# Kernel tuning notes

Hardware: AMD Instinct MI355X
Metric: run time of the kernel (lower is better)

The kernel has to match this reference:

```python
import jax, jax.numpy as jnp
import numpy as np

HEADS = 4
KNN = 32
N_KEYS = 512
K_DIM = 512
HALF = K_DIM // 2
V_DIM = 1024
IN_DIM = 1024


def setup_inputs() -> dict:
    key = jax.random.key(0)
    k1, k2, k3, k4, k5 = jax.random.split(key, 5)
    x = jax.random.normal(k1, (1, 2048, IN_DIM), dtype=jnp.float32)
    w_q = jax.random.normal(k2, (HEADS * K_DIM, IN_DIM), dtype=jnp.float32) * (IN_DIM ** -0.5)
    b_q = jax.random.normal(k3, (HEADS * K_DIM,), dtype=jnp.float32) * 0.01
    # subkeys: uniform(-1/sqrt(half), 1/sqrt(half)) as in get_uniform_keys
    bound = 1.0 / np.sqrt(HALF)
    keys = jax.random.uniform(k4, (HEADS, 2, N_KEYS, HALF), dtype=jnp.float32,
                              minval=-bound, maxval=bound)
    # values: normal(0, v_dim**-0.5)
    values = jax.random.normal(k5, (N_KEYS * N_KEYS, V_DIM), dtype=jnp.float32) * (V_DIM ** -0.5)
    return {"x": x, "w_q": w_q, "b_q": b_q, "keys": keys, "values": values}


def reference(x, w_q, b_q, keys, values):
    B, S, D = x.shape
    bs = B * S
    # query projection: (bs, heads*k_dim) -> (bs, heads, 2, half)
    q = (x.reshape(bs, D) @ w_q.T + b_q).reshape(bs, HEADS, 2, HALF)
    # per-head, per-half subkey scores: (bs, heads, 2, n_keys)
    scores = jnp.einsum('bhtd,htnd->bhtn', q, keys)
    s_top, i_top = jax.lax.top_k(scores, KNN)          # (bs, heads, 2, knn)
    s1, s2 = s_top[:, :, 0], s_top[:, :, 1]
    i1, i2 = i_top[:, :, 0], i_top[:, :, 1]
    # cross-product of the two half top-k sets: (bs, heads, knn*knn)
    all_s = (s1[..., :, None] + s2[..., None, :]).reshape(bs, HEADS, KNN * KNN)
    all_i = (i1[..., :, None] * N_KEYS + i2[..., None, :]).reshape(bs, HEADS, KNN * KNN)
    best_s, best_pos = jax.lax.top_k(all_s, KNN)       # (bs, heads, knn)
    idx = jnp.take_along_axis(all_i, best_pos, axis=-1)
    # softmax over knn per head (matches softmax on scores.view(-1, knn))
    w = jax.nn.softmax(best_s, axis=-1).reshape(bs, HEADS * KNN)
    idx = idx.reshape(bs, HEADS * KNN)
    # weighted EmbeddingBag gather-sum over the value table
    out = jnp.einsum('bk,bkd->bd', w, values[idx])     # (bs, v_dim)
    return out.reshape(B, S, V_DIM)
```

## Files before the change

### kernel.cpp

```cpp
#include <hip/hip_runtime.h>
#include <math.h>

#define BSZ   2048
#define INDIM 1024
#define QDIM  2048
#define NHT   8
#define NKEYS 512
#define HALFD 256
#define KNN   32
#define VDIM  1024
#define HEADS 4

typedef _Float16 v8h __attribute__((ext_vector_type(8)));
typedef _Float16 v4h __attribute__((ext_vector_type(4)));
typedef float    v4f __attribute__((ext_vector_type(4)));

template<int KSHIFT, bool ASIDE>
__global__ __launch_bounds__(256) void split_kernel(
    const float* __restrict__ in, _Float16* __restrict__ out, int total4) {
  const int i = blockIdx.x * 256 + threadIdx.x;
  if (i >= total4) return;
  const long e0 = (long)i * 4;
  const int K = 1 << KSHIFT;
  const long r = e0 >> KSHIFT;
  const int k = (int)(e0 & (K - 1));
  const float4 a = *(const float4*)&in[e0];
  const float av[4] = {a.x, a.y, a.z, a.w};
  v4h hv, dv, mv;
  #pragma unroll
  for (int u = 0; u < 4; ++u) {
    const _Float16 hh = (_Float16)av[u];
    hv[u] = hh;
    mv[u] = (_Float16)((av[u] - (float)hh) * 64.0f);
    dv[u] = (_Float16)((float)hh * 0.015625f);
  }
  _Float16* base = out + r * (3L * K) + k;
  *(v4h*)(base)         = hv;
  *(v4h*)(base + K)     = ASIDE ? dv : mv;
  *(v4h*)(base + 2 * K) = ASIDE ? mv : dv;
}

__device__ __forceinline__ void gload16(const _Float16* g, _Float16* l) {
  __builtin_amdgcn_global_load_lds(
      (const __attribute__((address_space(1))) unsigned int*)g,
      (__attribute__((address_space(3))) unsigned int*)l, 16, 0, 0);
}

template<bool Q_EPI>
__global__ __launch_bounds__(256) void mfma_gemm(
    const _Float16* __restrict__ A, int lda, long aBS,
    const _Float16* __restrict__ B, int ldb, long bBS,
    const float* __restrict__ bias,
    float* __restrict__ Cf, int ldc, long cBS,
    _Float16* __restrict__ Cq, int K) {
  extern __shared__ __align__(16) char smem[];
  _Float16* Asm = (_Float16*)smem;
  _Float16* Bsm = (_Float16*)(smem + 16384);
  const int t = threadIdx.x;
  const int z = blockIdx.z;
  const _Float16* Ab = A + (size_t)z * aBS;
  const _Float16* Bb = B + (size_t)z * bBS;
  const int m0 = blockIdx.y * 128, n0 = blockIdx.x * 128;

  const int o0 = t * 16;
  const int os = o0 ^ (((o0 >> 7) & 3) << 4);
  const int sr = os >> 6;
  const int sk = (os & 63) >> 1;
  const _Float16* gA0 = Ab + (size_t)(m0 + sr) * lda + sk;
  const _Float16* gA1 = Ab + (size_t)(m0 + sr + 64) * lda + sk;
  const _Float16* gB0 = Bb + (size_t)(n0 + sr) * ldb + sk;
  const _Float16* gB1 = Bb + (size_t)(n0 + sr + 64) * ldb + sk;

  const int lane = t & 63, w = t >> 6;
  const int wr = (w >> 1) * 64, wc = (w & 1) * 64;
  const int fr = lane & 15, kg = lane >> 4;

  int aoff[4], boff[4];
  #pragma unroll
  for (int i = 0; i < 4; ++i) {
    const int ra = wr + i * 16 + fr;
    aoff[i] = (ra * 64 + ((kg ^ ((ra >> 1) & 3)) * 16)) >> 1;
    const int rb = wc + i * 16 + fr;
    boff[i] = (rb * 64 + ((kg ^ ((rb >> 1) & 3)) * 16)) >> 1;
  }

  v4f acc[4][4];
  #pragma unroll
  for (int i = 0; i < 4; ++i)
    #pragma unroll
    for (int j = 0; j < 4; ++j)
      acc[i][j] = (v4f){0.f, 0.f, 0.f, 0.f};

  gload16(gA0, Asm + t * 8);
  gload16(gA1, Asm + 2048 + t * 8);
  gload16(gB0, Bsm + t * 8);
  gload16(gB1, Bsm + 2048 + t * 8);
  __syncthreads();

  int cur = 0;
  for (int kt = 0; kt < K; kt += 32) {
    const int nxt = cur ^ 1;
    if (kt + 32 < K) {
      gload16(gA0 + kt + 32, Asm + nxt * 4096 + t * 8);
      gload16(gA1 + kt + 32, Asm + nxt * 4096 + 2048 + t * 8);
      gload16(gB0 + kt + 32, Bsm + nxt * 4096 + t * 8);
      gload16(gB1 + kt + 32, Bsm + nxt * 4096 + 2048 + t * 8);
    }
    v8h af[4], bf[4];
    #pragma unroll
    for (int i = 0; i < 4; ++i) af[i] = *(const v8h*)(Asm + cur * 4096 + aoff[i]);
    #pragma unroll
    for (int j = 0; j < 4; ++j) bf[j] = *(const v8h*)(Bsm + cur * 4096 + boff[j]);
    #pragma unroll
    for (int i = 0; i < 4; ++i)
      #pragma unroll
      for (int j = 0; j < 4; ++j)
        acc[i][j] = __builtin_amdgcn_mfma_f32_16x16x32_f16(af[i], bf[j], acc[i][j], 0, 0, 0);
    __syncthreads();
    cur = nxt;
  }

  if (Q_EPI) {
    float* Ct = (float*)smem;
    #pragma unroll
    for (int half = 0; half < 2; ++half) {
      __syncthreads();
      if ((w & 1) == half) {
        #pragma unroll
        for (int j = 0; j < 4; ++j) {
          const int colq = j * 16 + fr;
          const float bv = bias[n0 + half * 64 + colq];
          #pragma unroll
          for (int i = 0; i < 4; ++i)
            #pragma unroll
            for (int rr = 0; rr < 4; ++rr)
              Ct[(wr + i * 16 + kg * 4 + rr) * 68 + colq] = acc[i][j][rr] + bv;
        }
      }
      __syncthreads();
      const int r = t >> 1, cb = (t & 1) * 32;
      const int gcol = n0 + half * 64 + cb;
      const int ht = gcol >> 8, dd = gcol & 255;
      _Float16* p = Cq + (size_t)(m0 + r) * (3 * HALFD * NHT) + ht * (3 * HALFD) + dd;
      #pragma unroll
      for (int u = 0; u < 32; u += 8) {
        float vv[8];
        *(float4*)&vv[0] = *(const float4*)&Ct[r * 68 + cb + u];
        *(float4*)&vv[4] = *(const float4*)&Ct[r * 68 + cb + u + 4];
        v8h hv, dv, mv;
        #pragma unroll
        for (int e = 0; e < 8; ++e) {
          const _Float16 hh = (_Float16)vv[e];
          hv[e] = hh;
          mv[e] = (_Float16)((vv[e] - (float)hh) * 64.0f);
          dv[e] = (_Float16)((float)hh * 0.015625f);
        }
        *(v8h*)(p + u) = hv;
        *(v8h*)(p + HALFD + u) = dv;
        *(v8h*)(p + 2 * HALFD + u) = mv;
      }
    }
  } else {
    float* Cb = Cf + (size_t)z * cBS;
    #pragma unroll
    for (int i = 0; i < 4; ++i)
      #pragma unroll
      for (int j = 0; j < 4; ++j)
        #pragma unroll
        for (int rr = 0; rr < 4; ++rr) {
          const int rowg = m0 + wr + i * 16 + kg * 4 + rr;
          const int colg = n0 + wc + j * 16 + fr;
          Cb[(size_t)rowg * ldc + colg] = acc[i][j][rr];
        }
  }
}

__global__ __launch_bounds__(64) void topk1_kernel(
    const float* __restrict__ S, float* __restrict__ sTop, int* __restrict__ iTop) {
  const int row = blockIdx.x;
  const int lane = threadIdx.x;
  const float* sr = S + (size_t)row * NKEYS;
  float v[8];
  #pragma unroll
  for (int j = 0; j < 8; ++j) v[j] = sr[j * 64 + lane];
  for (int r = 0; r < KNN; ++r) {
    float bv = -INFINITY; int bi = 0x7fffffff;
    #pragma unroll
    for (int j = 0; j < 8; ++j) {
      int idx = j * 64 + lane;
      if (v[j] > bv) { bv = v[j]; bi = idx; }
    }
    #pragma unroll
    for (int off = 32; off > 0; off >>= 1) {
      float ov = __shfl_xor(bv, off);
      int oi = __shfl_xor(bi, off);
      if (ov > bv || (ov == bv && oi < bi)) { bv = ov; bi = oi; }
    }
    if (lane == 0) { sTop[(size_t)row * KNN + r] = bv; iTop[(size_t)row * KNN + r] = bi; }
    const int jj = bi >> 6;
    const bool mine = (bi & 63) == lane;
    #pragma unroll
    for (int j = 0; j < 8; ++j)
      if (mine && j == jj) v[j] = -INFINITY;
  }
}

__global__ __launch_bounds__(64) void topk2_kernel(
    const float* __restrict__ sTop, const int* __restrict__ iTop,
    float* __restrict__ wOut, int* __restrict__ idxOut) {
  const int row = blockIdx.x;
  const int lane = threadIdx.x;
  __shared__ float ls1[32], ls2[32], sel_s[32];
  __shared__ int li1[32], li2[32], sel_i[32];
  if (lane < 32) {
    ls1[lane] = sTop[(size_t)(2 * row) * KNN + lane];
    li1[lane] = iTop[(size_t)(2 * row) * KNN + lane];
    ls2[lane] = sTop[(size_t)(2 * row + 1) * KNN + lane];
    li2[lane] = iTop[(size_t)(2 * row + 1) * KNN + lane];
  }
  __syncthreads();
  float v[16];
  #pragma unroll
  for (int c = 0; c < 16; ++c) {
    int p = c * 64 + lane;
    v[c] = ls1[p >> 5] + ls2[p & 31];
  }
  for (int r = 0; r < KNN; ++r) {
    float bv = -INFINITY; int bp = 0x7fffffff;
    #pragma unroll
    for (int c = 0; c < 16; ++c) {
      int p = c * 64 + lane;
      if (v[c] > bv) { bv = v[c]; bp = p; }
    }
    #pragma unroll
    for (int off = 32; off > 0; off >>= 1) {
      float ov = __shfl_xor(bv, off);
      int op = __shfl_xor(bp, off);
      if (ov > bv || (ov == bv && op < bp)) { bv = ov; bp = op; }
    }
    if (lane == 0) {
      sel_s[r] = bv;
      sel_i[r] = li1[bp >> 5] * NKEYS + li2[bp & 31];
    }
    const int cc = bp >> 6;
    const bool mine = (bp & 63) == lane;
    #pragma unroll
    for (int c = 0; c < 16; ++c)
      if (mine && c == cc) v[c] = -INFINITY;
  }
  __syncthreads();
  const float m = sel_s[0];
  float e = (lane < 32) ? expf(sel_s[lane] - m) : 0.0f;
  float s = e;
  #pragma unroll
  for (int off = 32; off > 0; off >>= 1) s += __shfl_xor(s, off);
  if (lane < 32) {
    wOut[(size_t)row * KNN + lane] = e / s;
    idxOut[(size_t)row * KNN + lane] = sel_i[lane];
  }
}

__global__ __launch_bounds__(256) void gather_kernel(
    const float* __restrict__ values, const float* __restrict__ w,
    const int* __restrict__ idx, float* __restrict__ out) {
  const int b = blockIdx.x;
  const int tid = threadIdx.x;
  __shared__ float lw[128];
  __shared__ int lidx[128];
  if (tid < 128) {
    lw[tid] = w[(size_t)b * 128 + tid];
    lidx[tid] = idx[(size_t)b * 128 + tid];
  }
  __syncthreads();
  const int d0 = tid * 4;
  float4 acc = {0.f, 0.f, 0.f, 0.f};
  #pragma unroll 8
  for (int k = 0; k < 128; ++k) {
    const float4 vv = *(const float4*)&values[(size_t)lidx[k] * VDIM + d0];
    const float ww = lw[k];
    acc.x = fmaf(ww, vv.x, acc.x);
    acc.y = fmaf(ww, vv.y, acc.y);
    acc.z = fmaf(ww, vv.z, acc.z);
    acc.w = fmaf(ww, vv.w, acc.w);
  }
  *(float4*)&out[(size_t)b * VDIM + d0] = acc;
}

extern "C" void kernel_launch(void* const* d_in, const int* in_sizes, int n_in,
                              void* d_out, int out_size, void* d_ws, size_t ws_size,
                              hipStream_t stream) {
  const float* x      = (const float*)d_in[0];
  const float* w_q    = (const float*)d_in[1];
  const float* b_q    = (const float*)d_in[2];
  const float* keys   = (const float*)d_in[3];
  const float* values = (const float*)d_in[4];
  float* out = (float*)d_out;

  char* ws = (char*)d_ws;
  _Float16* xs    = (_Float16*)(ws);
  _Float16* wqs   = (_Float16*)(ws + (16u  << 20));
  _Float16* keyss = (_Float16*)(ws + (32u  << 20));
  _Float16* Qs    = (_Float16*)(ws + (40u  << 20));
  float*    S     = (float*)   (ws + (68u  << 20));
  float*    sTop  = (float*)   (ws + (100u << 20));
  int*      iTop  = (int*)     (ws + (102u << 20));
  float*    wF    = (float*)   (ws + (104u << 20));
  int*      idxF  = (int*)     (ws + (105u << 20));

  split_kernel<10, true ><<<2048, 256, 0, stream>>>(x,    xs,    524288);
  split_kernel<10, false><<<2048, 256, 0, stream>>>(w_q,  wqs,   524288);
  split_kernel<8,  false><<<1024, 256, 0, stream>>>(keys, keyss, 262144);

  mfma_gemm<true><<<dim3(QDIM / 128, BSZ / 128, 1), 256, 34816, stream>>>(
      xs, 3 * INDIM, 0, wqs, 3 * INDIM, 0, b_q,
      nullptr, 0, 0, Qs, 3 * INDIM);
  mfma_gemm<false><<<dim3(NKEYS / 128, BSZ / 128, NHT), 256, 32768, stream>>>(
      Qs, 3 * HALFD * NHT, 3 * HALFD, keyss, 3 * HALFD, (long)NKEYS * 3 * HALFD, nullptr,
      S, NHT * NKEYS, NKEYS, nullptr, 3 * HALFD);

  topk1_kernel<<<BSZ * NHT, 64, 0, stream>>>(S, sTop, iTop);
  topk2_kernel<<<BSZ * HEADS, 64, 0, stream>>>(sTop, iTop, wF, idxF);
  gather_kernel<<<BSZ, 256, 0, stream>>>(values, wF, idxF, out);
}
```

Measured before the change: 412.6 us.

## Fuse splits, widen GEMM K-tile, fuse score GEMM with top-k and top-k2 with gather

Merges the three fp16 split launches into one kernel. The query GEMM moves to a 64-wide K tile with an 8-way swizzle. The score GEMM becomes a 64x512 tile per block whose results stay in LDS and feed a per-row top-k there, so the full score matrix is never written to or read back from global memory. The second top-k, softmax and weighted gather now run in one kernel per token with four heads per block. This cuts launches and intermediate traffic, at the cost of very large LDS use (over 144 KB per block), which limits occupancy in the fused score kernel.

Result: slower. 468.1 us (+13.4%).

```diff
diff --git a/kernel.cpp b/kernel.cpp
--- a/kernel.cpp
+++ b/kernel.cpp
@@ -16,10 +16,8 @@
 typedef float    v4f __attribute__((ext_vector_type(4)));
 
 template<int KSHIFT, bool ASIDE>
-__global__ __launch_bounds__(256) void split_kernel(
-    const float* __restrict__ in, _Float16* __restrict__ out, int total4) {
-  const int i = blockIdx.x * 256 + threadIdx.x;
-  if (i >= total4) return;
+__device__ __forceinline__ void split4(const float* __restrict__ in,
+                                       _Float16* __restrict__ out, int i) {
   const long e0 = (long)i * 4;
   const int K = 1 << KSHIFT;
   const long r = e0 >> KSHIFT;
@@ -40,49 +38,55 @@
   *(v4h*)(base + 2 * K) = ASIDE ? mv : dv;
 }
 
+__global__ __launch_bounds__(256) void split_all_kernel(
+    const float* __restrict__ x, const float* __restrict__ wq, const float* __restrict__ ky,
+    _Float16* __restrict__ xs, _Float16* __restrict__ wqs, _Float16* __restrict__ kys) {
+  const int i = blockIdx.x * 256 + threadIdx.x;
+  if (i < 524288)            split4<10, true >(x,  xs,  i);
+  else if (i < 1048576)      split4<10, false>(wq, wqs, i - 524288);
+  else                       split4<8,  false>(ky, kys, i - 1048576);
+}
+
 __device__ __forceinline__ void gload16(const _Float16* g, _Float16* l) {
   __builtin_amdgcn_global_load_lds(
       (const __attribute__((address_space(1))) unsigned int*)g,
       (__attribute__((address_space(3))) unsigned int*)l, 16, 0, 0);
 }
 
-template<bool Q_EPI>
-__global__ __launch_bounds__(256) void mfma_gemm(
-    const _Float16* __restrict__ A, int lda, long aBS,
-    const _Float16* __restrict__ B, int ldb, long bBS,
-    const float* __restrict__ bias,
-    float* __restrict__ Cf, int ldc, long cBS,
-    _Float16* __restrict__ Cq, int K) {
-  extern __shared__ __align__(16) char smem[];
-  _Float16* Asm = (_Float16*)smem;
-  _Float16* Bsm = (_Float16*)(smem + 16384);
+__global__ __launch_bounds__(256) void gemm1_kernel(
+    const _Float16* __restrict__ A, const _Float16* __restrict__ B,
+    const float* __restrict__ bias, _Float16* __restrict__ Cq) {
+  __shared__ __align__(16) char smem[65536];
+  _Float16* sh = (_Float16*)smem;
   const int t = threadIdx.x;
-  const int z = blockIdx.z;
-  const _Float16* Ab = A + (size_t)z * aBS;
-  const _Float16* Bb = B + (size_t)z * bBS;
   const int m0 = blockIdx.y * 128, n0 = blockIdx.x * 128;
-
-  const int o0 = t * 16;
-  const int os = o0 ^ (((o0 >> 7) & 3) << 4);
-  const int sr = os >> 6;
-  const int sk = (os & 63) >> 1;
-  const _Float16* gA0 = Ab + (size_t)(m0 + sr) * lda + sk;
-  const _Float16* gA1 = Ab + (size_t)(m0 + sr + 64) * lda + sk;
-  const _Float16* gB0 = Bb + (size_t)(n0 + sr) * ldb + sk;
-  const _Float16* gB1 = Bb + (size_t)(n0 + sr + 64) * ldb + sk;
-
   const int lane = t & 63, w = t >> 6;
   const int wr = (w >> 1) * 64, wc = (w & 1) * 64;
   const int fr = lane & 15, kg = lane >> 4;
 
-  int aoff[4], boff[4];
-  #pragma unroll
-  for (int i = 0; i < 4; ++i) {
-    const int ra = wr + i * 16 + fr;
-    aoff[i] = (ra * 64 + ((kg ^ ((ra >> 1) & 3)) * 16)) >> 1;
-    const int rb = wc + i * 16 + fr;
-    boff[i] = (rb * 64 + ((kg ^ ((rb >> 1) & 3)) * 16)) >> 1;
-  }
+  const _Float16* gA[4]; const _Float16* gB[4];
+  int dA[4], dB[4];
+  #pragma unroll
+  for (int p = 0; p < 4; ++p) {
+    const int O = p * 4096 + t * 16;
+    const int os = O ^ (((O >> 7) & 7) << 4);
+    const int srow = os >> 7, sk = (os & 127) >> 1;
+    gA[p] = A + (size_t)(m0 + srow) * 3072 + sk;
+    gB[p] = B + (size_t)(n0 + srow) * 3072 + sk;
+    dA[p] = O >> 1;
+    dB[p] = (16384 + O) >> 1;
+  }
+
+  int aof[2][4], bof[2][4];
+  #pragma unroll
+  for (int ks = 0; ks < 2; ++ks)
+    #pragma unroll
+    for (int i = 0; i < 4; ++i) {
+      const int ra = wr + i * 16 + fr;
+      aof[ks][i] = (ra * 128 + ((((ks << 2) | kg) ^ (fr & 7)) << 4)) >> 1;
+      const int rb = wc + i * 16 + fr;
+      bof[ks][i] = ((rb * 128 + ((((ks << 2) | kg) ^ (fr & 7)) << 4)) >> 1) + 8192;
+    }
 
   v4f acc[4][4];
   #pragma unroll
@@ -91,156 +95,236 @@
     for (int j = 0; j < 4; ++j)
       acc[i][j] = (v4f){0.f, 0.f, 0.f, 0.f};
 
-  gload16(gA0, Asm + t * 8);
-  gload16(gA1, Asm + 2048 + t * 8);
-  gload16(gB0, Bsm + t * 8);
-  gload16(gB1, Bsm + 2048 + t * 8);
+  #pragma unroll
+  for (int p = 0; p < 4; ++p) { gload16(gA[p], sh + dA[p]); gload16(gB[p], sh + dB[p]); }
   __syncthreads();
 
   int cur = 0;
-  for (int kt = 0; kt < K; kt += 32) {
-    const int nxt = cur ^ 1;
-    if (kt + 32 < K) {
-      gload16(gA0 + kt + 32, Asm + nxt * 4096 + t * 8);
-      gload16(gA1 + kt + 32, Asm + nxt * 4096 + 2048 + t * 8);
-      gload16(gB0 + kt + 32, Bsm + nxt * 4096 + t * 8);
-      gload16(gB1 + kt + 32, Bsm + nxt * 4096 + 2048 + t * 8);
-    }
-    v8h af[4], bf[4];
-    #pragma unroll
-    for (int i = 0; i < 4; ++i) af[i] = *(const v8h*)(Asm + cur * 4096 + aoff[i]);
-    #pragma unroll
-    for (int j = 0; j < 4; ++j) bf[j] = *(const v8h*)(Bsm + cur * 4096 + boff[j]);
-    #pragma unroll
-    for (int i = 0; i < 4; ++i)
-      #pragma unroll
-      for (int j = 0; j < 4; ++j)
-        acc[i][j] = __builtin_amdgcn_mfma_f32_16x16x32_f16(af[i], bf[j], acc[i][j], 0, 0, 0);
+  for (int kt = 0; kt < 3072; kt += 64) {
+    if (kt + 64 < 3072) {
+      _Float16* bb = sh + (cur ^ 1) * 16384;
+      #pragma unroll
+      for (int p = 0; p < 4; ++p) {
+        gload16(gA[p] + kt + 64, bb + dA[p]);
+        gload16(gB[p] + kt + 64, bb + dB[p]);
+      }
+    }
+    const _Float16* bb = sh + cur * 16384;
+    #pragma unroll
+    for (int ks = 0; ks < 2; ++ks) {
+      v8h af[4], bf[4];
+      #pragma unroll
+      for (int i = 0; i < 4; ++i) af[i] = *(const v8h*)(bb + aof[ks][i]);
+      #pragma unroll
+      for (int j = 0; j < 4; ++j) bf[j] = *(const v8h*)(bb + bof[ks][j]);
+      #pragma unroll
+      for (int i = 0; i < 4; ++i)
+        #pragma unroll
+        for (int j = 0; j < 4; ++j)
+          acc[i][j] = __builtin_amdgcn_mfma_f32_16x16x32_f16(af[i], bf[j], acc[i][j], 0, 0, 0);
+    }
     __syncthreads();
-    cur = nxt;
-  }
-
-  if (Q_EPI) {
-    float* Ct = (float*)smem;
-    #pragma unroll
-    for (int half = 0; half < 2; ++half) {
-      __syncthreads();
-      if ((w & 1) == half) {
+    cur ^= 1;
+  }
+
+  float* Ct = (float*)smem;
+  #pragma unroll
+  for (int half = 0; half < 2; ++half) {
+    __syncthreads();
+    if ((w & 1) == half) {
+      #pragma unroll
+      for (int j = 0; j < 4; ++j) {
+        const int colq = j * 16 + fr;
+        const float bv = bias[n0 + half * 64 + colq];
         #pragma unroll
-        for (int j = 0; j < 4; ++j) {
-          const int colq = j * 16 + fr;
-          const float bv = bias[n0 + half * 64 + colq];
+        for (int i = 0; i < 4; ++i)
           #pragma unroll
-          for (int i = 0; i < 4; ++i)
-            #pragma unroll
-            for (int rr = 0; rr < 4; ++rr)
-              Ct[(wr + i * 16 + kg * 4 + rr) * 68 + colq] = acc[i][j][rr] + bv;
-        }
-      }
-      __syncthreads();
-      const int r = t >> 1, cb = (t & 1) * 32;
-      const int gcol = n0 + half * 64 + cb;
-      const int ht = gcol >> 8, dd = gcol & 255;
-      _Float16* p = Cq + (size_t)(m0 + r) * (3 * HALFD * NHT) + ht * (3 * HALFD) + dd;
-      #pragma unroll
-      for (int u = 0; u < 32; u += 8) {
-        float vv[8];
-        *(float4*)&vv[0] = *(const float4*)&Ct[r * 68 + cb + u];
-        *(float4*)&vv[4] = *(const float4*)&Ct[r * 68 + cb + u + 4];
-        v8h hv, dv, mv;
+          for (int rr = 0; rr < 4; ++rr)
+            Ct[(wr + i * 16 + kg * 4 + rr) * 68 + colq] = acc[i][j][rr] + bv;
+      }
+    }
+    __syncthreads();
+    const int r = t >> 1, cb = (t & 1) * 32;
+    const int gcol = n0 + half * 64 + cb;
+    const int ht = gcol >> 8, dd = gcol & 255;
+    _Float16* p = Cq + (size_t)(m0 + r) * (3 * HALFD * NHT) + ht * (3 * HALFD) + dd;
+    #pragma unroll
+    for (int u = 0; u < 32; u += 8) {
+      float vv[8];
+      *(float4*)&vv[0] = *(const float4*)&Ct[r * 68 + cb + u];
+      *(float4*)&vv[4] = *(const float4*)&Ct[r * 68 + cb + u + 4];
+      v8h hv, dv, mv;
+      #pragma unroll
+      for (int e = 0; e < 8; ++e) {
+        const _Float16 hh = (_Float16)vv[e];
+        hv[e] = hh;
+        mv[e] = (_Float16)((vv[e] - (float)hh) * 64.0f);
+        dv[e] = (_Float16)((float)hh * 0.015625f);
+      }
+      *(v8h*)(p + u) = hv;
+      *(v8h*)(p + HALFD + u) = dv;
+      *(v8h*)(p + 2 * HALFD + u) = mv;
+    }
+  }
+}
+
+__global__ __launch_bounds__(512) void gemm2_topk_kernel(
+    const _Float16* __restrict__ Qs, const _Float16* __restrict__ Ks,
+    float* __restrict__ sTop, int* __restrict__ iTop) {
+  __shared__ __align__(16) char smem[147456];
+  __shared__ float sels[8][32];
+  __shared__ int   seli[8][32];
+  _Float16* sh = (_Float16*)smem;
+  const int t = threadIdx.x;
+  const int m0 = blockIdx.x * 64;
+  const int ht = blockIdx.y;
+  const _Float16* Ab = Qs + (size_t)ht * 768;
+  const _Float16* Bb = Ks + (size_t)ht * 512 * 768;
+  const int lane = t & 63, w = t >> 6;
+  const int fr = lane & 15, kg = lane >> 4;
+  const int wc = w * 64;
+
+  const int OA = t * 16;
+  const int osA = OA ^ (((OA >> 7) & 7) << 4);
+  const _Float16* gA = Ab + (size_t)(m0 + (osA >> 7)) * 6144 + ((osA & 127) >> 1);
+  const int dA = OA >> 1;
+  const _Float16* gB[8]; int dB[8];
+  #pragma unroll
+  for (int p = 0; p < 8; ++p) {
+    const int O = p * 8192 + t * 16;
+    const int os = O ^ (((O >> 7) & 7) << 4);
+    gB[p] = Bb + (size_t)(os >> 7) * 768 + ((os & 127) >> 1);
+    dB[p] = (8192 + O) >> 1;
+  }
+
+  int aof[2][4], bof[2][4];
+  #pragma unroll
+  for (int ks = 0; ks < 2; ++ks)
+    #pragma unroll
+    for (int i = 0; i < 4; ++i) {
+      const int ra = i * 16 + fr;
+      aof[ks][i] = (ra * 128 + ((((ks << 2) | kg) ^ (fr & 7)) << 4)) >> 1;
+      const int rb = wc + i * 16 + fr;
+      bof[ks][i] = ((rb * 128 + ((((ks << 2) | kg) ^ (fr & 7)) << 4)) >> 1) + 4096;
+    }
+
+  v4f acc[4][4];
+  #pragma unroll
+  for (int i = 0; i < 4; ++i)
+    #pragma unroll
+    for (int j = 0; j < 4; ++j)
+      acc[i][j] = (v4f){0.f, 0.f, 0.f, 0.f};
+
+  gload16(gA, sh + dA);
+  #pragma unroll
+  for (int p = 0; p < 8; ++p) gload16(gB[p], sh + dB[p]);
+  __syncthreads();
+
+  int cur = 0;
+  for (int kt = 0; kt < 768; kt += 64) {
+    if (kt + 64 < 768) {
+      _Float16* bb = sh + (cur ^ 1) * 36864;
+      gload16(gA + kt + 64, bb + dA);
+      #pragma unroll
+      for (int p = 0; p < 8; ++p) gload16(gB[p] + kt + 64, bb + dB[p]);
+    }
+    const _Float16* bb = sh + cur * 36864;
+    #pragma unroll
+    for (int ks = 0; ks < 2; ++ks) {
+      v8h af[4], bf[4];
+      #pragma unroll
+      for (int i = 0; i < 4; ++i) af[i] = *(const v8h*)(bb + aof[ks][i]);
+      #pragma unroll
+      for (int j = 0; j < 4; ++j) bf[j] = *(const v8h*)(bb + bof[ks][j]);
+      #pragma unroll
+      for (int i = 0; i < 4; ++i)
         #pragma unroll
-        for (int e = 0; e < 8; ++e) {
-          const _Float16 hh = (_Float16)vv[e];
-          hv[e] = hh;
-          mv[e] = (_Float16)((vv[e] - (float)hh) * 64.0f);
-          dv[e] = (_Float16)((float)hh * 0.015625f);
-        }
-        *(v8h*)(p + u) = hv;
-        *(v8h*)(p + HALFD + u) = dv;
-        *(v8h*)(p + 2 * HALFD + u) = mv;
-      }
-    }
-  } else {
-    float* Cb = Cf + (size_t)z * cBS;
-    #pragma unroll
-    for (int i = 0; i < 4; ++i)
-      #pragma unroll
-      for (int j = 0; j < 4; ++j)
-        #pragma unroll
-        for (int rr = 0; rr < 4; ++rr) {
-          const int rowg = m0 + wr + i * 16 + kg * 4 + rr;
-          const int colg = n0 + wc + j * 16 + fr;
-          Cb[(size_t)rowg * ldc + colg] = acc[i][j][rr];
-        }
-  }
-}
-
-__global__ __launch_bounds__(64) void topk1_kernel(
-    const float* __restrict__ S, float* __restrict__ sTop, int* __restrict__ iTop) {
-  const int row = blockIdx.x;
-  const int lane = threadIdx.x;
-  const float* sr = S + (size_t)row * NKEYS;
-  float v[8];
-  #pragma unroll
-  for (int j = 0; j < 8; ++j) v[j] = sr[j * 64 + lane];
-  for (int r = 0; r < KNN; ++r) {
-    float bv = -INFINITY; int bi = 0x7fffffff;
-    #pragma unroll
-    for (int j = 0; j < 8; ++j) {
-      int idx = j * 64 + lane;
-      if (v[j] > bv) { bv = v[j]; bi = idx; }
-    }
-    #pragma unroll
-    for (int off = 32; off > 0; off >>= 1) {
-      float ov = __shfl_xor(bv, off);
-      int oi = __shfl_xor(bi, off);
-      if (ov > bv || (ov == bv && oi < bi)) { bv = ov; bi = oi; }
-    }
-    if (lane == 0) { sTop[(size_t)row * KNN + r] = bv; iTop[(size_t)row * KNN + r] = bi; }
-    const int jj = bi >> 6;
-    const bool mine = (bi & 63) == lane;
-    #pragma unroll
-    for (int j = 0; j < 8; ++j)
-      if (mine && j == jj) v[j] = -INFINITY;
-  }
-}
-
-__global__ __launch_bounds__(64) void topk2_kernel(
+        for (int j = 0; j < 4; ++j)
+          acc[i][j] = __builtin_amdgcn_mfma_f32_16x16x32_f16(af[i], bf[j], acc[i][j], 0, 0, 0);
+    }
+    __syncthreads();
+    cur ^= 1;
+  }
+
+  float* Sl = (float*)smem;
+  #pragma unroll
+  for (int i = 0; i < 4; ++i)
+    #pragma unroll
+    for (int j = 0; j < 4; ++j)
+      #pragma unroll
+      for (int rr = 0; rr < 4; ++rr)
+        Sl[(i * 16 + kg * 4 + rr) * 516 + wc + j * 16 + fr] = acc[i][j][rr];
+  __syncthreads();
+
+  for (int rw = 0; rw < 8; ++rw) {
+    const int row = w * 8 + rw;
+    float v[8];
+    #pragma unroll
+    for (int jj = 0; jj < 8; ++jj) v[jj] = Sl[row * 516 + jj * 64 + lane];
+    for (int r = 0; r < KNN; ++r) {
+      float bv = -INFINITY; int bi = 0x7fffffff;
+      #pragma unroll
+      for (int jj = 0; jj < 8; ++jj) {
+        const int idx = jj * 64 + lane;
+        if (v[jj] > bv) { bv = v[jj]; bi = idx; }
+      }
+      #pragma unroll
+      for (int off = 32; off > 0; off >>= 1) {
+        const float ov = __shfl_xor(bv, off);
+        const int oi = __shfl_xor(bi, off);
+        if (ov > bv || (ov == bv && oi < bi)) { bv = ov; bi = oi; }
+      }
+      if (lane == 0) { sels[w][r] = bv; seli[w][r] = bi; }
+      const int jj0 = bi >> 6;
+      const bool mine = (bi & 63) == lane;
+      #pragma unroll
+      for (int jj = 0; jj < 8; ++jj)
+        if (mine && jj == jj0) v[jj] = -INFINITY;
+    }
+    if (lane < 32) {
+      const size_t ro = ((size_t)(m0 + row) * NHT + ht) * KNN;
+      sTop[ro + lane] = sels[w][lane];
+      iTop[ro + lane] = seli[w][lane];
+    }
+  }
+}
+
+__global__ __launch_bounds__(256) void topk2_gather_kernel(
     const float* __restrict__ sTop, const int* __restrict__ iTop,
-    float* __restrict__ wOut, int* __restrict__ idxOut) {
-  const int row = blockIdx.x;
-  const int lane = threadIdx.x;
-  __shared__ float ls1[32], ls2[32], sel_s[32];
-  __shared__ int li1[32], li2[32], sel_i[32];
+    const float* __restrict__ values, float* __restrict__ out) {
+  __shared__ float ls1[4][32], ls2[4][32], sels[4][32];
+  __shared__ int   li1[4][32], li2[4][32], seli[4][32];
+  __shared__ float lw[128];
+  __shared__ int   lidx[128];
+  const int b = blockIdx.x, t = threadIdx.x;
+  const int lane = t & 63, h = t >> 6;
+  const size_t r1 = ((size_t)b * NHT + 2 * h) * KNN;
   if (lane < 32) {
-    ls1[lane] = sTop[(size_t)(2 * row) * KNN + lane];
-    li1[lane] = iTop[(size_t)(2 * row) * KNN + lane];
-    ls2[lane] = sTop[(size_t)(2 * row + 1) * KNN + lane];
-    li2[lane] = iTop[(size_t)(2 * row + 1) * KNN + lane];
-  }
-  __syncthreads();
+    ls1[h][lane] = sTop[r1 + lane];        li1[h][lane] = iTop[r1 + lane];
+    ls2[h][lane] = sTop[r1 + KNN + lane];  li2[h][lane] = iTop[r1 + KNN + lane];
+  }
   float v[16];
   #pragma unroll
   for (int c = 0; c < 16; ++c) {
-    int p = c * 64 + lane;
-    v[c] = ls1[p >> 5] + ls2[p & 31];
+    const int p = c * 64 + lane;
+    v[c] = ls1[h][p >> 5] + ls2[h][p & 31];
   }
   for (int r = 0; r < KNN; ++r) {
     float bv = -INFINITY; int bp = 0x7fffffff;
     #pragma unroll
     for (int c = 0; c < 16; ++c) {
-      int p = c * 64 + lane;
+      const int p = c * 64 + lane;
       if (v[c] > bv) { bv = v[c]; bp = p; }
     }
     #pragma unroll
     for (int off = 32; off > 0; off >>= 1) {
-      float ov = __shfl_xor(bv, off);
-      int op = __shfl_xor(bp, off);
+      const float ov = __shfl_xor(bv, off);
+      const int op = __shfl_xor(bp, off);
       if (ov > bv || (ov == bv && op < bp)) { bv = ov; bp = op; }
     }
     if (lane == 0) {
-      sel_s[r] = bv;
-      sel_i[r] = li1[bp >> 5] * NKEYS + li2[bp & 31];
+      sels[h][r] = bv;
+      seli[h][r] = li1[h][bp >> 5] * NKEYS + li2[h][bp & 31];
     }
     const int cc = bp >> 6;
     const bool mine = (bp & 63) == lane;
@@ -248,31 +332,17 @@
     for (int c = 0; c < 16; ++c)
       if (mine && c == cc) v[c] = -INFINITY;
   }
-  __syncthreads();
-  const float m = sel_s[0];
-  float e = (lane < 32) ? expf(sel_s[lane] - m) : 0.0f;
+  const float m = sels[h][0];
+  const float e = (lane < 32) ? expf(sels[h][lane] - m) : 0.0f;
   float s = e;
   #pragma unroll
   for (int off = 32; off > 0; off >>= 1) s += __shfl_xor(s, off);
   if (lane < 32) {
-    wOut[(size_t)row * KNN + lane] = e / s;
-    idxOut[(size_t)row * KNN + lane] = sel_i[lane];
-  }
-}
-
-__global__ __launch_bounds__(256) void gather_kernel(
-    const float* __restrict__ values, const float* __restrict__ w,
-    const int* __restrict__ idx, float* __restrict__ out) {
-  const int b = blockIdx.x;
-  const int tid = threadIdx.x;
-  __shared__ float lw[128];
-  __shared__ int lidx[128];
-  if (tid < 128) {
-    lw[tid] = w[(size_t)b * 128 + tid];
-    lidx[tid] = idx[(size_t)b * 128 + tid];
+    lw[h * 32 + lane] = e / s;
+    lidx[h * 32 + lane] = seli[h][lane];
   }
   __syncthreads();
-  const int d0 = tid * 4;
+  const int d0 = t * 4;
   float4 acc = {0.f, 0.f, 0.f, 0.f};
   #pragma unroll 8
   for (int k = 0; k < 128; ++k) {
@@ -298,27 +368,14 @@
 
   char* ws = (char*)d_ws;
   _Float16* xs    = (_Float16*)(ws);
-  _Float16* wqs   = (_Float16*)(ws + (16u  << 20));
-  _Float16* keyss = (_Float16*)(ws + (32u  << 20));
-  _Float16* Qs    = (_Float16*)(ws + (40u  << 20));
-  float*    S     = (float*)   (ws + (68u  << 20));
-  float*    sTop  = (float*)   (ws + (100u << 20));
-  int*      iTop  = (int*)     (ws + (102u << 20));
-  float*    wF    = (float*)   (ws + (104u << 20));
-  int*      idxF  = (int*)     (ws + (105u << 20));
-
-  split_kernel<10, true ><<<2048, 256, 0, stream>>>(x,    xs,    524288);
-  split_kernel<10, false><<<2048, 256, 0, stream>>>(w_q,  wqs,   524288);
-  split_kernel<8,  false><<<1024, 256, 0, stream>>>(keys, keyss, 262144);
-
-  mfma_gemm<true><<<dim3(QDIM / 128, BSZ / 128, 1), 256, 34816, stream>>>(
-      xs, 3 * INDIM, 0, wqs, 3 * INDIM, 0, b_q,
-      nullptr, 0, 0, Qs, 3 * INDIM);
-  mfma_gemm<false><<<dim3(NKEYS / 128, BSZ / 128, NHT), 256, 32768, stream>>>(
-      Qs, 3 * HALFD * NHT, 3 * HALFD, keyss, 3 * HALFD, (long)NKEYS * 3 * HALFD, nullptr,
-      S, NHT * NKEYS, NKEYS, nullptr, 3 * HALFD);
-
-  topk1_kernel<<<BSZ * NHT, 64, 0, stream>>>(S, sTop, iTop);
-  topk2_kernel<<<BSZ * HEADS, 64, 0, stream>>>(sTop, iTop, wF, idxF);
-  gather_kernel<<<BSZ, 256, 0, stream>>>(values, wF, idxF, out);
-}
+  _Float16* wqs   = (_Float16*)(ws + (16u << 20));
+  _Float16* keyss = (_Float16*)(ws + (32u << 20));
+  _Float16* Qs    = (_Float16*)(ws + (40u << 20));
+  float*    sTop  = (float*)   (ws + (68u << 20));
+  int*      iTop  = (int*)     (ws + (70u << 20));
+
+  split_all_kernel<<<5120, 256, 0, stream>>>(x, w_q, keys, xs, wqs, keyss);
+  gemm1_kernel<<<dim3(QDIM / 128, BSZ / 128), 256, 0, stream>>>(xs, wqs, b_q, Qs);
+  gemm2_topk_kernel<<<dim3(BSZ / 64, NHT), 512, 0, stream>>>(Qs, keyss, sTop, iTop);
+  topk2_gather_kernel<<<BSZ, 256, 0, stream>>>(sTop, iTop, values, out);
+}
```
